# Kernel tuning notes

Measured on AMD Instinct MI355X. Metric: run time of the kernel, lower is better.

The kernel has to match this reference:

```python
import jax, jax.numpy as jnp
import numpy as np

LN_EPS = 1e-5
NORM_EPS = 1e-12


def channel_layernorm(x, w, b):
    # LayerNorm over channel dim of NCHW tensor (torch permutes to NHWC; equivalent)
    mu = x.mean(axis=1, keepdims=True)
    var = x.var(axis=1, keepdims=True)
    xn = (x - mu) / jnp.sqrt(var + LN_EPS)
    return xn * w[None, :, None, None] + b[None, :, None, None]


def pconv(x, w):
    # 1x1 pointwise conv, w: (out_ch, in_ch)
    return jnp.einsum('bchw,oc->bohw', x, w)


def dwconv3(x, w):
    # depthwise 3x3, padding 1; w: (ch, 1, 3, 3)
    return jax.lax.conv_general_dilated(
        x, w, window_strides=(1, 1), padding='SAME',
        feature_group_count=x.shape[1],
        dimension_numbers=('NCHW', 'OIHW', 'NCHW'))


def l2norm(x):
    n = jnp.sqrt(jnp.sum(x * x, axis=-1, keepdims=True))
    return x / jnp.maximum(n, NORM_EPS)


def setup_inputs() -> dict:
    key = jax.random.key(0)
    ks = jax.random.split(key, 8)
    B, C, H, W = 4, 128, 128, 128
    NH, G = 8, 2

    def w(k, shape, fan_in):
        return jax.random.normal(k, shape, dtype=jnp.float32) * (fan_in ** -0.5)

    return {
        'x': jax.random.normal(ks[0], (B, C, H, W), dtype=jnp.float32),
        'ln1_w': jnp.ones((C,), jnp.float32),
        'ln1_b': jnp.zeros((C,), jnp.float32),
        'temperature': jnp.ones((NH, 1, 1), jnp.float32),
        'qkv_p_w': w(ks[1], (3 * C, C), C),
        'qkv_d_w': w(ks[2], (3 * C, 1, 3, 3), 9),
        'proj_w': w(ks[3], (C, C), C),
        'ln2_w': jnp.ones((C,), jnp.float32),
        'ln2_b': jnp.zeros((C,), jnp.float32),
        'g1_w': w(ks[4], (2 * G * C, C), C),
        'gd_w': w(ks[5], (2 * G * C, 1, 3, 3), 9),
        'g2_w': w(ks[6], (C, G * C), G * C),
        'num_heads': NH,
    }


def reference(x, ln1_w, ln1_b, temperature, qkv_p_w, qkv_d_w, proj_w,
              ln2_w, ln2_b, g1_w, gd_w, g2_w, num_heads):
    b, c, h, w_ = x.shape
    d = c // num_heads

    # --- MDTA branch ---
    y = channel_layernorm(x, ln1_w, ln1_b)
    qkv = dwconv3(pconv(y, qkv_p_w), qkv_d_w)  # (b, 3c, h, w)
    q, k, v = jnp.split(qkv, 3, axis=1)
    q = l2norm(q.reshape(b, num_heads, d, h * w_))
    k = l2norm(k.reshape(b, num_heads, d, h * w_))
    v = v.reshape(b, num_heads, d, h * w_)
    # transposed (channel) attention: (b, heads, d, d)
    attn = jnp.einsum('bhdn,bhen->bhde', q, k) * temperature[None]
    attn = jax.nn.softmax(attn, axis=-1)
    out = jnp.einsum('bhde,bhen->bhdn', attn, v).reshape(b, c, h, w_)
    x = x + pconv(out, proj_w)

    # --- GDFN branch ---
    y = channel_layernorm(x, ln2_w, ln2_b)
    hdn = dwconv3(pconv(y, g1_w), gd_w)  # (b, 2*gamma*c, h, w)
    x1, x2 = jnp.split(hdn, 2, axis=1)
    g = jax.nn.gelu(x1, approximate=False) * x2
    x = x + pconv(g, g2_w)
    return x
```

## Files before the change

kernel.cpp:

```cpp
#include <hip/hip_runtime.h>
#include <cstdint>
#include <cstddef>

typedef float f32x4 __attribute__((ext_vector_type(4)));
typedef __bf16 bf16x8 __attribute__((ext_vector_type(8)));

__device__ __forceinline__ float b2f(unsigned short u) {
    union { unsigned int i; float f; } z; z.i = ((unsigned int)u) << 16; return z.f;
}
__device__ __forceinline__ unsigned short f2b(float f) {
    union { float f; unsigned int i; } z; z.f = f;
    unsigned int x = z.i;
    return (unsigned short)((x + 0x7FFFu + ((x >> 16) & 1u)) >> 16);
}

static constexpr int C = 128;
static constexpr int NP = 16384;
static constexpr int NH = 8;

struct Ptr11 { const float* p[11]; };
__constant__ int kWN[11]   = {128, 128, 8, 49152, 3456, 16384, 128, 128, 65536, 4608, 32768};
__constant__ int kWOff[11] = {0, 128, 256, 272, 49424, 52880, 69264, 69392, 69520, 135056, 139664};
static constexpr int kWTotal = 172432;

__global__ __launch_bounds__(256)
void cvt_w_kernel(Ptr11 P, unsigned short* __restrict__ dst)
{
    int seg = blockIdx.y;
    int n = kWN[seg];
    int i = blockIdx.x * 256 + threadIdx.x;
    if (i >= n) return;
    dst[kWOff[seg] + i] = f2b(P.p[seg][i]);
}

__global__ __launch_bounds__(256)
void ln_kernel(const float* __restrict__ x, const unsigned short* __restrict__ g,
               const unsigned short* __restrict__ beta, unsigned short* __restrict__ y)
{
    int wave = threadIdx.x >> 6;
    int lane = threadIdx.x & 63;
    int px   = lane & 15;
    int cgrp = lane >> 4;
    int pglob = blockIdx.x * 64 + wave * 16 + px;
    int b = pglob >> 14;
    int n = pglob & (NP - 1);
    const float* xb = x + (size_t)b * C * NP + n;

    float vals[32];
    float s = 0.f, s2 = 0.f;
    #pragma unroll
    for (int i = 0; i < 32; ++i) {
        float v = xb[(size_t)(cgrp + 4 * i) * NP];
        vals[i] = v;
        s += v; s2 += v * v;
    }
    s  += __shfl_xor(s, 16, 64);  s2 += __shfl_xor(s2, 16, 64);
    s  += __shfl_xor(s, 32, 64);  s2 += __shfl_xor(s2, 32, 64);
    float mu = s * (1.0f / C);
    float var = s2 * (1.0f / C) - mu * mu;
    float rs = rsqrtf(fmaxf(var, 0.f) + 1e-5f);

    unsigned short* yb = y + (size_t)b * C * NP + n;
    #pragma unroll
    for (int i = 0; i < 32; ++i) {
        int c = cgrp + 4 * i;
        float o = (vals[i] - mu) * rs * b2f(g[c]) + b2f(beta[c]);
        yb[(size_t)c * NP] = f2b(o);
    }
}

template <int K, int EPI>
__global__ __launch_bounds__(256)
void gemm_pconv(const unsigned short* __restrict__ W,
                const unsigned short* __restrict__ X,
                void* __restrict__ Out,
                const float* __restrict__ Res,
                int Cout)
{
    __shared__ unsigned short Bs[32][128];
    const int tid = threadIdx.x;
    const int b = blockIdx.z;
    const int n0 = blockIdx.x * 128;
    const int m0 = blockIdx.y * 128;
    const unsigned short* Xb = X + (size_t)b * K * NP;
    const int wid = tid >> 6;
    const int lane = tid & 63;
    const int ln16 = lane & 15;
    const int quad = lane >> 4;
    const int wy = wid >> 1;
    const int wx = wid & 1;

    f32x4 acc[4][4];
    #pragma unroll
    for (int i = 0; i < 4; ++i)
        #pragma unroll
        for (int j = 0; j < 4; ++j)
            acc[i][j] = f32x4{0.f, 0.f, 0.f, 0.f};

    for (int k0 = 0; k0 < K; k0 += 32) {
        #pragma unroll
        for (int r = 0; r < 2; ++r) {
            int flat = tid + r * 256;
            int kk = flat >> 4;
            int nn = (flat & 15) * 8;
            uint4 v = *(const uint4*)(Xb + (size_t)(k0 + kk) * NP + n0 + nn);
            *(uint4*)(&Bs[kk][nn]) = v;
        }
        __syncthreads();

        bf16x8 afr[4];
        #pragma unroll
        for (int mt = 0; mt < 4; ++mt) {
            int m = m0 + wy * 64 + mt * 16 + ln16;
            uint4 v = *(const uint4*)(W + (size_t)m * K + k0 + quad * 8);
            afr[mt] = *(bf16x8*)&v;
        }
        bf16x8 bfr[4];
        #pragma unroll
        for (int nt = 0; nt < 4; ++nt) {
            int n = wx * 64 + nt * 16 + ln16;
            union { bf16x8 v; unsigned short u[8]; } tmp;
            #pragma unroll
            for (int j = 0; j < 8; ++j) tmp.u[j] = Bs[quad * 8 + j][n];
            bfr[nt] = tmp.v;
        }
        #pragma unroll
        for (int mt = 0; mt < 4; ++mt)
            #pragma unroll
            for (int nt = 0; nt < 4; ++nt)
                acc[mt][nt] = __builtin_amdgcn_mfma_f32_16x16x32_bf16(
                    afr[mt], bfr[nt], acc[mt][nt], 0, 0, 0);
        __syncthreads();
    }

    size_t outbase = (size_t)b * Cout * NP;
    #pragma unroll
    for (int mt = 0; mt < 4; ++mt) {
        #pragma unroll
        for (int nt = 0; nt < 4; ++nt) {
            int co0 = m0 + wy * 64 + mt * 16 + quad * 4;
            int n = n0 + wx * 64 + nt * 16 + ln16;
            #pragma unroll
            for (int r = 0; r < 4; ++r) {
                float v = acc[mt][nt][r];
                size_t idx = outbase + (size_t)(co0 + r) * NP + n;
                if (EPI == 0) ((unsigned short*)Out)[idx] = f2b(v);
                else          ((float*)Out)[idx] = Res[idx] + v;
            }
        }
    }
}

__global__ __launch_bounds__(256)
void dwconv3_kernel(const unsigned short* __restrict__ in,
                    const unsigned short* __restrict__ w9,
                    unsigned short* __restrict__ out, int CH)
{
    int t = blockIdx.x * 256 + threadIdx.x;
    int xi = (t & 15) * 8;
    int y  = (t >> 4) & 127;
    int bc = t >> 11;
    int c  = bc % CH;
    const unsigned short* base = in + (size_t)bc * NP + y * 128 + xi;

    float wr[9];
    #pragma unroll
    for (int i = 0; i < 9; ++i) wr[i] = b2f(w9[c * 9 + i]);

    uint4 rv0 = uint4{0,0,0,0}, rv1, rv2 = uint4{0,0,0,0};
    if (y > 0)   rv0 = *(const uint4*)(base - 128);
    rv1 = *(const uint4*)(base);
    if (y < 127) rv2 = *(const uint4*)(base + 128);
    uint4 rows[3] = {rv0, rv1, rv2};

    float o[8];
    #pragma unroll
    for (int j = 0; j < 8; ++j) o[j] = 0.f;

    #pragma unroll
    for (int r = 0; r < 3; ++r) {
        union { uint4 v; unsigned short u[8]; } cv; cv.v = rows[r];
        int lh = __shfl_up((int)cv.u[7], 1, 16);
        int rh = __shfl_down((int)cv.u[0], 1, 16);
        float p[10];
        p[0] = (xi > 0)   ? b2f((unsigned short)lh) : 0.f;
        p[9] = (xi < 120) ? b2f((unsigned short)rh) : 0.f;
        #pragma unroll
        for (int j = 0; j < 8; ++j) p[j + 1] = b2f(cv.u[j]);
        #pragma unroll
        for (int j = 0; j < 8; ++j)
            o[j] += wr[r * 3] * p[j] + wr[r * 3 + 1] * p[j + 1] + wr[r * 3 + 2] * p[j + 2];
    }
    union { uint4 v; unsigned short u[8]; } res;
    #pragma unroll
    for (int j = 0; j < 8; ++j) res.u[j] = f2b(o[j]);
    *(uint4*)(out + (size_t)bc * NP + y * 128 + xi) = res.v;
}

__global__ __launch_bounds__(256)
void dwgelu_kernel(const unsigned short* __restrict__ hdn,
                   const unsigned short* __restrict__ w9,
                   unsigned short* __restrict__ g)
{
    int t = blockIdx.x * 256 + threadIdx.x;
    int xi = (t & 15) * 8;
    int y  = (t >> 4) & 127;
    int bc = t >> 11;
    int c  = bc & 255;
    int b  = bc >> 8;
    const unsigned short* base1 = hdn + ((size_t)b * 512 + c) * NP + y * 128 + xi;
    const unsigned short* base2 = base1 + (size_t)256 * NP;

    float w1[9], w2[9];
    #pragma unroll
    for (int i = 0; i < 9; ++i) {
        w1[i] = b2f(w9[c * 9 + i]);
        w2[i] = b2f(w9[(c + 256) * 9 + i]);
    }

    uint4 ra0 = uint4{0,0,0,0}, ra1, ra2 = uint4{0,0,0,0};
    uint4 rb0 = uint4{0,0,0,0}, rb1, rb2 = uint4{0,0,0,0};
    if (y > 0)   { ra0 = *(const uint4*)(base1 - 128); rb0 = *(const uint4*)(base2 - 128); }
    ra1 = *(const uint4*)(base1);
    rb1 = *(const uint4*)(base2);
    if (y < 127) { ra2 = *(const uint4*)(base1 + 128); rb2 = *(const uint4*)(base2 + 128); }
    uint4 rowsA[3] = {ra0, ra1, ra2};
    uint4 rowsB[3] = {rb0, rb1, rb2};

    float a1[8], a2[8];
    #pragma unroll
    for (int j = 0; j < 8; ++j) { a1[j] = 0.f; a2[j] = 0.f; }

    #pragma unroll
    for (int r = 0; r < 3; ++r) {
        union { uint4 v; unsigned short u[8]; } c1, c2;
        c1.v = rowsA[r]; c2.v = rowsB[r];
        int lh1 = __shfl_up((int)c1.u[7], 1, 16);
        int rh1 = __shfl_down((int)c1.u[0], 1, 16);
        int lh2 = __shfl_up((int)c2.u[7], 1, 16);
        int rh2 = __shfl_down((int)c2.u[0], 1, 16);
        float p1[10], p2[10];
        p1[0] = (xi > 0)   ? b2f((unsigned short)lh1) : 0.f;
        p1[9] = (xi < 120) ? b2f((unsigned short)rh1) : 0.f;
        p2[0] = (xi > 0)   ? b2f((unsigned short)lh2) : 0.f;
        p2[9] = (xi < 120) ? b2f((unsigned short)rh2) : 0.f;
        #pragma unroll
        for (int j = 0; j < 8; ++j) { p1[j + 1] = b2f(c1.u[j]); p2[j + 1] = b2f(c2.u[j]); }
        #pragma unroll
        for (int j = 0; j < 8; ++j) {
            a1[j] += w1[r * 3] * p1[j] + w1[r * 3 + 1] * p1[j + 1] + w1[r * 3 + 2] * p1[j + 2];
            a2[j] += w2[r * 3] * p2[j] + w2[r * 3 + 1] * p2[j + 1] + w2[r * 3 + 2] * p2[j + 2];
        }
    }
    union { uint4 v; unsigned short u[8]; } res;
    #pragma unroll
    for (int j = 0; j < 8; ++j) {
        float u = a1[j];
        float tt = u * (0.7978845608f + 0.0356774081f * u * u);
        float e = __expf(2.f * tt);
        float th = 1.f - 2.f / (e + 1.f);
        float ge = 0.5f * u * (1.f + th);
        res.u[j] = f2b(ge * a2[j]);
    }
    *(uint4*)(g + (size_t)bc * NP + y * 128 + xi) = res.v;
}

__global__ __launch_bounds__(256)
void sumsq_kernel(const unsigned short* __restrict__ qkv, float* __restrict__ norms)
{
    int ch = blockIdx.x;
    int b = blockIdx.y;
    const unsigned short* p = qkv + ((size_t)b * 384 + ch) * NP;
    float s = 0.f;
    for (int i = threadIdx.x * 8; i < NP; i += 2048) {
        union { uint4 v; unsigned short u[8]; } cv;
        cv.v = *(const uint4*)(p + i);
        #pragma unroll
        for (int j = 0; j < 8; ++j) { float v = b2f(cv.u[j]); s += v * v; }
    }
    #pragma unroll
    for (int o = 32; o > 0; o >>= 1) s += __shfl_down(s, o, 64);
    __shared__ float ws4[4];
    if ((threadIdx.x & 63) == 0) ws4[threadIdx.x >> 6] = s;
    __syncthreads();
    if (threadIdx.x == 0) {
        float t = ws4[0] + ws4[1] + ws4[2] + ws4[3];
        norms[b * 256 + ch] = fmaxf(sqrtf(t), 1e-12f);
    }
}

__global__ __launch_bounds__(256)
void gram_kernel(const unsigned short* __restrict__ qkv, float* __restrict__ Spart)
{
    int h = blockIdx.x, b = blockIdx.y, sp = blockIdx.z;
    int wid = threadIdx.x >> 6, lane = threadIdx.x & 63;
    int ln16 = lane & 15, quad = lane >> 4;
    int nbase = sp * 2048 + wid * 512;
    const unsigned short* qp = qkv + ((size_t)b * 384 + h * 16 + ln16) * NP;
    const unsigned short* kp = qkv + ((size_t)b * 384 + 128 + h * 16 + ln16) * NP;
    f32x4 acc = f32x4{0.f, 0.f, 0.f, 0.f};
    for (int i = 0; i < 512; i += 32) {
        int n = nbase + i + quad * 8;
        uint4 av = *(const uint4*)(qp + n);
        uint4 bv = *(const uint4*)(kp + n);
        acc = __builtin_amdgcn_mfma_f32_16x16x32_bf16(*(bf16x8*)&av, *(bf16x8*)&bv, acc, 0, 0, 0);
    }
    float* Sp = Spart + (((size_t)(b * NH + h) * 32) + sp * 4 + wid) * 256;
    #pragma unroll
    for (int r = 0; r < 4; ++r)
        Sp[(quad * 4 + r) * 16 + ln16] = acc[r];
}

__global__ __launch_bounds__(256)
void softmax_kernel(const float* __restrict__ Spart, const float* __restrict__ norms,
                    const unsigned short* __restrict__ temp, float* __restrict__ P)
{
    int bh = blockIdx.x;
    int b = bh >> 3, h = bh & 7;
    int t = threadIdx.x;
    int dq = t >> 4, dk = t & 15;
    float sacc = 0.f;
    const float* Sp = Spart + (size_t)bh * 32 * 256;
    #pragma unroll
    for (int j = 0; j < 32; ++j) sacc += Sp[j * 256 + t];
    float nq = norms[b * 256 + h * 16 + dq];
    float nk = norms[b * 256 + 128 + h * 16 + dk];
    float v = sacc / (nq * nk) * b2f(temp[h]);
    float m = v;
    #pragma unroll
    for (int o = 8; o > 0; o >>= 1) m = fmaxf(m, __shfl_xor(m, o, 16));
    float e = __expf(v - m);
    float s = e;
    #pragma unroll
    for (int o = 8; o > 0; o >>= 1) s += __shfl_xor(s, o, 16);
    P[(size_t)bh * 256 + t] = e / s;
}

__global__ __launch_bounds__(256)
void attnv_kernel(const float* __restrict__ P, const unsigned short* __restrict__ qkv,
                  unsigned short* __restrict__ out)
{
    __shared__ float Ps[256];
    int h = blockIdx.y, b = blockIdx.z;
    Ps[threadIdx.x] = P[((size_t)b * NH + h) * 256 + threadIdx.x];
    __syncthreads();
    int n = (blockIdx.x * 256 + threadIdx.x) * 4;
    const unsigned short* vp = qkv + ((size_t)b * 384 + 256 + h * 16) * NP + n;
    float o[16][4];
    #pragma unroll
    for (int d = 0; d < 16; ++d)
        #pragma unroll
        for (int j = 0; j < 4; ++j) o[d][j] = 0.f;
    #pragma unroll
    for (int e = 0; e < 16; ++e) {
        union { uint2 v; unsigned short u[4]; } cv;
        cv.v = *(const uint2*)(vp + (size_t)e * NP);
        float v0 = b2f(cv.u[0]), v1 = b2f(cv.u[1]), v2 = b2f(cv.u[2]), v3 = b2f(cv.u[3]);
        #pragma unroll
        for (int d = 0; d < 16; ++d) {
            float p = Ps[d * 16 + e];
            o[d][0] += p * v0; o[d][1] += p * v1; o[d][2] += p * v2; o[d][3] += p * v3;
        }
    }
    unsigned short* op = out + ((size_t)b * C + h * 16) * NP + n;
    #pragma unroll
    for (int d = 0; d < 16; ++d) {
        union { uint2 v; unsigned short u[4]; } res;
        #pragma unroll
        for (int j = 0; j < 4; ++j) res.u[j] = f2b(o[d][j]);
        *(uint2*)(op + (size_t)d * NP) = res.v;
    }
}

struct Bufs {
    float* xmid;
    unsigned short* y;
    unsigned short* big;
    unsigned short* mid;
    float* norms;
    float* Spart;
    float* P;
};

static void run_pipeline(const float* x_f32, float* out_f32,
                         const unsigned short* w,
                         const Bufs& B, int nb, hipStream_t stream)
{
    const unsigned short* ln1_w   = w + 0;
    const unsigned short* ln1_b   = w + 128;
    const unsigned short* temp    = w + 256;
    const unsigned short* qkv_p_w = w + 272;
    const unsigned short* qkv_d_w = w + 49424;
    const unsigned short* proj_w  = w + 52880;
    const unsigned short* ln2_w   = w + 69264;
    const unsigned short* ln2_b   = w + 69392;
    const unsigned short* g1_w    = w + 69520;
    const unsigned short* gd_w    = w + 135056;
    const unsigned short* g2_w    = w + 139664;

    ln_kernel<<<nb * NP / 64, 256, 0, stream>>>(x_f32, ln1_w, ln1_b, B.y);
    gemm_pconv<128, 0><<<dim3(NP / 128, 3, nb), 256, 0, stream>>>(qkv_p_w, B.y, B.big, nullptr, 384);
    dwconv3_kernel<<<nb * 384 * NP / 2048, 256, 0, stream>>>(B.big, qkv_d_w, B.mid, 384);
    sumsq_kernel<<<dim3(256, nb), 256, 0, stream>>>(B.mid, B.norms);
    gram_kernel<<<dim3(NH, nb, 8), 256, 0, stream>>>(B.mid, B.Spart);
    softmax_kernel<<<nb * NH, 256, 0, stream>>>(B.Spart, B.norms, temp, B.P);
    attnv_kernel<<<dim3(NP / 1024, NH, nb), 256, 0, stream>>>(B.P, B.mid, B.y);
    gemm_pconv<128, 1><<<dim3(NP / 128, 1, nb), 256, 0, stream>>>(proj_w, B.y, B.xmid, x_f32, 128);

    ln_kernel<<<nb * NP / 64, 256, 0, stream>>>(B.xmid, ln2_w, ln2_b, B.y);
    gemm_pconv<128, 0><<<dim3(NP / 128, 4, nb), 256, 0, stream>>>(g1_w, B.y, B.big, nullptr, 512);
    dwgelu_kernel<<<nb * 256 * NP / 2048, 256, 0, stream>>>(B.big, gd_w, B.mid);
    gemm_pconv<256, 1><<<dim3(NP / 128, 1, nb), 256, 0, stream>>>(g2_w, B.mid, out_f32, B.xmid, 128);
}

extern "C" void kernel_launch(void* const* d_in, const int* in_sizes, int n_in,
                              void* d_out, int out_size, void* d_ws, size_t ws_size,
                              hipStream_t stream)
{
    (void)in_sizes; (void)n_in; (void)out_size;
    const float* x = (const float*)d_in[0];
    char* ws = (char*)d_ws;

    size_t off = 0;
    unsigned short* wpack = (unsigned short*)(ws + off);
    off += (size_t)kWTotal * 2;
    off = (off + 255) & ~(size_t)255;
    size_t header = off;

    auto layout = [&](int nb, size_t o, Bufs& B) -> size_t {
        B.xmid = (float*)(ws + o);           o += (size_t)nb * C * NP * 4;
        B.y    = (unsigned short*)(ws + o);  o += (size_t)nb * C * NP * 2;
        B.big  = (unsigned short*)(ws + o);  o += (size_t)nb * 512 * NP * 2;
        B.mid  = (unsigned short*)(ws + o);  o += (size_t)nb * 384 * NP * 2;
        B.norms = (float*)(ws + o);          o += (size_t)nb * 256 * 4;
        B.Spart = (float*)(ws + o);          o += (size_t)nb * NH * 32 * 256 * 4;
        B.P     = (float*)(ws + o);          o += (size_t)nb * NH * 256 * 4;
        return o;
    };

    Ptr11 P;
    for (int i = 0; i < 11; ++i) P.p[i] = (const float*)d_in[i + 1];
    cvt_w_kernel<<<dim3(256, 11), 256, 0, stream>>>(P, wpack);

    Bufs Bfull;
    size_t need_full = layout(4, header, Bfull);

    if (ws_size >= need_full) {
        run_pipeline(x, (float*)d_out, wpack, Bfull, 4, stream);
    } else {
        Bufs B1;
        layout(1, header, B1);
        for (int b = 0; b < 4; ++b) {
            run_pipeline(x + (size_t)b * C * NP,
                         (float*)d_out + (size_t)b * C * NP,
                         wpack, B1, 1, stream);
        }
    }
}
```

Before: 275.5 us.

## Switch LN and attention outputs to pixel-major layout and fuse sum-of-squares into dwconv

```diff
diff --git a/kernel.cpp b/kernel.cpp
--- a/kernel.cpp
+++ b/kernel.cpp
@@ -33,49 +33,147 @@
     dst[kWOff[seg] + i] = f2b(P.p[seg][i]);
 }
 
+__global__ void zero_kernel(float* __restrict__ p) { p[blockIdx.x * 256 + threadIdx.x] = 0.f; }
+
 __global__ __launch_bounds__(256)
 void ln_kernel(const float* __restrict__ x, const unsigned short* __restrict__ g,
                const unsigned short* __restrict__ beta, unsigned short* __restrict__ y)
 {
-    int wave = threadIdx.x >> 6;
-    int lane = threadIdx.x & 63;
-    int px   = lane & 15;
-    int cgrp = lane >> 4;
-    int pglob = blockIdx.x * 64 + wave * 16 + px;
+    int t = threadIdx.x;
+    int px = t & 15;
+    int tg = t >> 4;
+    int pglob = blockIdx.x * 16 + px;
     int b = pglob >> 14;
     int n = pglob & (NP - 1);
     const float* xb = x + (size_t)b * C * NP + n;
 
-    float vals[32];
-    float s = 0.f, s2 = 0.f;
-    #pragma unroll
-    for (int i = 0; i < 32; ++i) {
-        float v = xb[(size_t)(cgrp + 4 * i) * NP];
-        vals[i] = v;
-        s += v; s2 += v * v;
+    float v[8]; float s = 0.f, s2 = 0.f;
+    #pragma unroll
+    for (int i = 0; i < 8; ++i) {
+        float w = xb[(size_t)(tg * 8 + i) * NP];
+        v[i] = w; s += w; s2 += w * w;
     }
     s  += __shfl_xor(s, 16, 64);  s2 += __shfl_xor(s2, 16, 64);
     s  += __shfl_xor(s, 32, 64);  s2 += __shfl_xor(s2, 32, 64);
-    float mu = s * (1.0f / C);
-    float var = s2 * (1.0f / C) - mu * mu;
+    __shared__ float sm[2][4][16];
+    if ((t & 63) < 16) { sm[0][t >> 6][px] = s; sm[1][t >> 6][px] = s2; }
+    __syncthreads();
+    float S  = sm[0][0][px] + sm[0][1][px] + sm[0][2][px] + sm[0][3][px];
+    float S2 = sm[1][0][px] + sm[1][1][px] + sm[1][2][px] + sm[1][3][px];
+    float mu = S * (1.0f / C);
+    float var = S2 * (1.0f / C) - mu * mu;
     float rs = rsqrtf(fmaxf(var, 0.f) + 1e-5f);
 
-    unsigned short* yb = y + (size_t)b * C * NP + n;
-    #pragma unroll
-    for (int i = 0; i < 32; ++i) {
-        int c = cgrp + 4 * i;
-        float o = (vals[i] - mu) * rs * b2f(g[c]) + b2f(beta[c]);
-        yb[(size_t)c * NP] = f2b(o);
-    }
+    union { uint4 q; unsigned short u[8]; } res;
+    #pragma unroll
+    for (int i = 0; i < 8; ++i) {
+        int c = tg * 8 + i;
+        res.u[i] = f2b((v[i] - mu) * rs * b2f(g[c]) + b2f(beta[c]));
+    }
+    *(uint4*)(y + (size_t)pglob * C + tg * 8) = res.q;
 }
 
 template <int K, int EPI>
 __global__ __launch_bounds__(256)
-void gemm_pconv(const unsigned short* __restrict__ W,
-                const unsigned short* __restrict__ X,
-                void* __restrict__ Out,
-                const float* __restrict__ Res,
-                int Cout)
+void gemm_nk(const unsigned short* __restrict__ W,
+             const unsigned short* __restrict__ X,
+             void* __restrict__ Out,
+             const float* __restrict__ Res,
+             int Cout)
+{
+    const int tid = threadIdx.x;
+    const int b = blockIdx.z;
+    const int n0 = blockIdx.x * 128;
+    const int co0 = blockIdx.y * 128;
+    const int lane = tid & 63;
+    const int wid = tid >> 6;
+    const int ln16 = lane & 15;
+    const int quad = lane >> 4;
+    const int wy = wid >> 1;
+    const int wx = wid & 1;
+    const unsigned short* Xb = X + ((size_t)b * NP + n0) * K;
+
+    f32x4 acc[4][4];
+    #pragma unroll
+    for (int i = 0; i < 4; ++i)
+        #pragma unroll
+        for (int j = 0; j < 4; ++j)
+            acc[i][j] = f32x4{0.f, 0.f, 0.f, 0.f};
+
+    #pragma unroll 2
+    for (int k0 = 0; k0 < K; k0 += 32) {
+        bf16x8 afr[4];
+        #pragma unroll
+        for (int mt = 0; mt < 4; ++mt) {
+            int row = wy * 64 + mt * 16 + ln16;
+            uint4 v = *(const uint4*)(Xb + (size_t)row * K + k0 + quad * 8);
+            afr[mt] = *(bf16x8*)&v;
+        }
+        bf16x8 bfr[4];
+        #pragma unroll
+        for (int nt = 0; nt < 4; ++nt) {
+            int co = co0 + wx * 64 + nt * 16 + ln16;
+            uint4 v = *(const uint4*)(W + (size_t)co * K + k0 + quad * 8);
+            bfr[nt] = *(bf16x8*)&v;
+        }
+        #pragma unroll
+        for (int mt = 0; mt < 4; ++mt)
+            #pragma unroll
+            for (int nt = 0; nt < 4; ++nt)
+                acc[mt][nt] = __builtin_amdgcn_mfma_f32_16x16x32_bf16(
+                    afr[mt], bfr[nt], acc[mt][nt], 0, 0, 0);
+    }
+
+    if constexpr (EPI == 0) {
+        __shared__ unsigned short Ts[128 * 136];
+        #pragma unroll
+        for (int mt = 0; mt < 4; ++mt) {
+            #pragma unroll
+            for (int nt = 0; nt < 4; ++nt) {
+                int co_l = wx * 64 + nt * 16 + ln16;
+                int n_l  = wy * 64 + mt * 16 + quad * 4;
+                union { uint2 d; unsigned short u[4]; } pk;
+                #pragma unroll
+                for (int r = 0; r < 4; ++r) pk.u[r] = f2b(acc[mt][nt][r]);
+                *(uint2*)&Ts[co_l * 136 + n_l] = pk.d;
+            }
+        }
+        __syncthreads();
+        unsigned short* ob = (unsigned short*)Out;
+        #pragma unroll
+        for (int i = 0; i < 8; ++i) {
+            int idx = tid + 256 * i;
+            int co_l = idx >> 4;
+            int oct  = idx & 15;
+            uint4 v = *(const uint4*)&Ts[co_l * 136 + oct * 8];
+            *(uint4*)(ob + (size_t)b * Cout * NP + (size_t)(co0 + co_l) * NP + n0 + oct * 8) = v;
+        }
+    } else {
+        float* ob = (float*)Out;
+        #pragma unroll
+        for (int mt = 0; mt < 4; ++mt) {
+            #pragma unroll
+            for (int nt = 0; nt < 4; ++nt) {
+                int co = co0 + wx * 64 + nt * 16 + ln16;
+                int n = n0 + wy * 64 + mt * 16 + quad * 4;
+                size_t idx = (size_t)b * Cout * NP + (size_t)co * NP + n;
+                f32x4 rv = *(const f32x4*)&Res[idx];
+                f32x4 ov;
+                #pragma unroll
+                for (int r = 0; r < 4; ++r) ov[r] = rv[r] + acc[mt][nt][r];
+                *(f32x4*)&ob[idx] = ov;
+            }
+        }
+    }
+}
+
+template <int K>
+__global__ __launch_bounds__(256)
+void gemm_cn(const unsigned short* __restrict__ W,
+             const unsigned short* __restrict__ X,
+             float* __restrict__ Out,
+             const float* __restrict__ Res,
+             int Cout)
 {
     __shared__ unsigned short Bs[32][128];
     const int tid = threadIdx.x;
@@ -133,7 +231,6 @@
         __syncthreads();
     }
 
-    size_t outbase = (size_t)b * Cout * NP;
     #pragma unroll
     for (int mt = 0; mt < 4; ++mt) {
         #pragma unroll
@@ -142,10 +239,8 @@
             int n = n0 + wx * 64 + nt * 16 + ln16;
             #pragma unroll
             for (int r = 0; r < 4; ++r) {
-                float v = acc[mt][nt][r];
-                size_t idx = outbase + (size_t)(co0 + r) * NP + n;
-                if (EPI == 0) ((unsigned short*)Out)[idx] = f2b(v);
-                else          ((float*)Out)[idx] = Res[idx] + v;
+                size_t idx = (size_t)b * Cout * NP + (size_t)(co0 + r) * NP + n;
+                Out[idx] = Res[idx] + acc[mt][nt][r];
             }
         }
     }
@@ -154,13 +249,15 @@
 __global__ __launch_bounds__(256)
 void dwconv3_kernel(const unsigned short* __restrict__ in,
                     const unsigned short* __restrict__ w9,
-                    unsigned short* __restrict__ out, int CH)
+                    unsigned short* __restrict__ out, int CH,
+                    float* __restrict__ norms2)
 {
     int t = blockIdx.x * 256 + threadIdx.x;
     int xi = (t & 15) * 8;
     int y  = (t >> 4) & 127;
     int bc = t >> 11;
     int c  = bc % CH;
+    int b  = bc / CH;
     const unsigned short* base = in + (size_t)bc * NP + y * 128 + xi;
 
     float wr[9];
@@ -192,9 +289,18 @@
             o[j] += wr[r * 3] * p[j] + wr[r * 3 + 1] * p[j + 1] + wr[r * 3 + 2] * p[j + 2];
     }
     union { uint4 v; unsigned short u[8]; } res;
-    #pragma unroll
-    for (int j = 0; j < 8; ++j) res.u[j] = f2b(o[j]);
+    float ss = 0.f;
+    #pragma unroll
+    for (int j = 0; j < 8; ++j) { res.u[j] = f2b(o[j]); ss += o[j] * o[j]; }
     *(uint4*)(out + (size_t)bc * NP + y * 128 + xi) = res.v;
+
+    #pragma unroll
+    for (int off = 32; off > 0; off >>= 1) ss += __shfl_down(ss, off, 64);
+    __shared__ float sred[4];
+    if ((threadIdx.x & 63) == 0) sred[threadIdx.x >> 6] = ss;
+    __syncthreads();
+    if (threadIdx.x == 0 && c < 256)
+        atomicAdd(&norms2[b * 256 + c], sred[0] + sred[1] + sred[2] + sred[3]);
 }
 
 __global__ __launch_bounds__(256)
@@ -259,34 +365,9 @@
         float tt = u * (0.7978845608f + 0.0356774081f * u * u);
         float e = __expf(2.f * tt);
         float th = 1.f - 2.f / (e + 1.f);
-        float ge = 0.5f * u * (1.f + th);
-        res.u[j] = f2b(ge * a2[j]);
+        res.u[j] = f2b(0.5f * u * (1.f + th) * a2[j]);
     }
     *(uint4*)(g + (size_t)bc * NP + y * 128 + xi) = res.v;
-}
-
-__global__ __launch_bounds__(256)
-void sumsq_kernel(const unsigned short* __restrict__ qkv, float* __restrict__ norms)
-{
-    int ch = blockIdx.x;
-    int b = blockIdx.y;
-    const unsigned short* p = qkv + ((size_t)b * 384 + ch) * NP;
-    float s = 0.f;
-    for (int i = threadIdx.x * 8; i < NP; i += 2048) {
-        union { uint4 v; unsigned short u[8]; } cv;
-        cv.v = *(const uint4*)(p + i);
-        #pragma unroll
-        for (int j = 0; j < 8; ++j) { float v = b2f(cv.u[j]); s += v * v; }
-    }
-    #pragma unroll
-    for (int o = 32; o > 0; o >>= 1) s += __shfl_down(s, o, 64);
-    __shared__ float ws4[4];
-    if ((threadIdx.x & 63) == 0) ws4[threadIdx.x >> 6] = s;
-    __syncthreads();
-    if (threadIdx.x == 0) {
-        float t = ws4[0] + ws4[1] + ws4[2] + ws4[3];
-        norms[b * 256 + ch] = fmaxf(sqrtf(t), 1e-12f);
-    }
 }
 
 __global__ __launch_bounds__(256)
@@ -312,7 +393,7 @@
 }
 
 __global__ __launch_bounds__(256)
-void softmax_kernel(const float* __restrict__ Spart, const float* __restrict__ norms,
+void softmax_kernel(const float* __restrict__ Spart, const float* __restrict__ norms2,
                     const unsigned short* __restrict__ temp, float* __restrict__ P)
 {
     int bh = blockIdx.x;
@@ -323,8 +404,8 @@
     const float* Sp = Spart + (size_t)bh * 32 * 256;
     #pragma unroll
     for (int j = 0; j < 32; ++j) sacc += Sp[j * 256 + t];
-    float nq = norms[b * 256 + h * 16 + dq];
-    float nk = norms[b * 256 + 128 + h * 16 + dk];
+    float nq = fmaxf(sqrtf(norms2[b * 256 + h * 16 + dq]), 1e-12f);
+    float nk = fmaxf(sqrtf(norms2[b * 256 + 128 + h * 16 + dk]), 1e-12f);
     float v = sacc / (nq * nk) * b2f(temp[h]);
     float m = v;
     #pragma unroll
@@ -344,8 +425,8 @@
     int h = blockIdx.y, b = blockIdx.z;
     Ps[threadIdx.x] = P[((size_t)b * NH + h) * 256 + threadIdx.x];
     __syncthreads();
-    int n = (blockIdx.x * 256 + threadIdx.x) * 4;
-    const unsigned short* vp = qkv + ((size_t)b * 384 + 256 + h * 16) * NP + n;
+    int n0 = (blockIdx.x * 256 + threadIdx.x) * 4;
+    const unsigned short* vp = qkv + ((size_t)b * 384 + 256 + h * 16) * NP + n0;
     float o[16][4];
     #pragma unroll
     for (int d = 0; d < 16; ++d)
@@ -362,13 +443,14 @@
             o[d][0] += p * v0; o[d][1] += p * v1; o[d][2] += p * v2; o[d][3] += p * v3;
         }
     }
-    unsigned short* op = out + ((size_t)b * C + h * 16) * NP + n;
-    #pragma unroll
-    for (int d = 0; d < 16; ++d) {
-        union { uint2 v; unsigned short u[4]; } res;
-        #pragma unroll
-        for (int j = 0; j < 4; ++j) res.u[j] = f2b(o[d][j]);
-        *(uint2*)(op + (size_t)d * NP) = res.v;
+    #pragma unroll
+    for (int j = 0; j < 4; ++j) {
+        union { uint4 q[2]; unsigned short u[16]; } res;
+        #pragma unroll
+        for (int d = 0; d < 16; ++d) res.u[d] = f2b(o[d][j]);
+        unsigned short* op = out + ((size_t)b * NP + n0 + j) * 128 + h * 16;
+        *(uint4*)op = res.q[0];
+        *(uint4*)(op + 8) = res.q[1];
     }
 }
 
@@ -377,14 +459,13 @@
     unsigned short* y;
     unsigned short* big;
     unsigned short* mid;
-    float* norms;
+    float* norms2;
     float* Spart;
     float* P;
 };
 
 static void run_pipeline(const float* x_f32, float* out_f32,
-                         const unsigned short* w,
-                         const Bufs& B, int nb, hipStream_t stream)
+                         const unsigned short* w, const Bufs& B, int nb, hipStream_t stream)
 {
     const unsigned short* ln1_w   = w + 0;
     const unsigned short* ln1_b   = w + 128;
@@ -398,19 +479,19 @@
     const unsigned short* gd_w    = w + 135056;
     const unsigned short* g2_w    = w + 139664;
 
-    ln_kernel<<<nb * NP / 64, 256, 0, stream>>>(x_f32, ln1_w, ln1_b, B.y);
-    gemm_pconv<128, 0><<<dim3(NP / 128, 3, nb), 256, 0, stream>>>(qkv_p_w, B.y, B.big, nullptr, 384);
-    dwconv3_kernel<<<nb * 384 * NP / 2048, 256, 0, stream>>>(B.big, qkv_d_w, B.mid, 384);
-    sumsq_kernel<<<dim3(256, nb), 256, 0, stream>>>(B.mid, B.norms);
+    ln_kernel<<<nb * NP / 16, 256, 0, stream>>>(x_f32, ln1_w, ln1_b, B.y);
+    gemm_nk<128, 0><<<dim3(NP / 128, 3, nb), 256, 0, stream>>>(qkv_p_w, B.y, B.big, nullptr, 384);
+    zero_kernel<<<nb, 256, 0, stream>>>(B.norms2);
+    dwconv3_kernel<<<nb * 384 * NP / 2048, 256, 0, stream>>>(B.big, qkv_d_w, B.mid, 384, B.norms2);
     gram_kernel<<<dim3(NH, nb, 8), 256, 0, stream>>>(B.mid, B.Spart);
-    softmax_kernel<<<nb * NH, 256, 0, stream>>>(B.Spart, B.norms, temp, B.P);
+    softmax_kernel<<<nb * NH, 256, 0, stream>>>(B.Spart, B.norms2, temp, B.P);
     attnv_kernel<<<dim3(NP / 1024, NH, nb), 256, 0, stream>>>(B.P, B.mid, B.y);
-    gemm_pconv<128, 1><<<dim3(NP / 128, 1, nb), 256, 0, stream>>>(proj_w, B.y, B.xmid, x_f32, 128);
-
-    ln_kernel<<<nb * NP / 64, 256, 0, stream>>>(B.xmid, ln2_w, ln2_b, B.y);
-    gemm_pconv<128, 0><<<dim3(NP / 128, 4, nb), 256, 0, stream>>>(g1_w, B.y, B.big, nullptr, 512);
+    gemm_nk<128, 1><<<dim3(NP / 128, 1, nb), 256, 0, stream>>>(proj_w, B.y, B.xmid, x_f32, 128);
+
+    ln_kernel<<<nb * NP / 16, 256, 0, stream>>>(B.xmid, ln2_w, ln2_b, B.y);
+    gemm_nk<128, 0><<<dim3(NP / 128, 4, nb), 256, 0, stream>>>(g1_w, B.y, B.big, nullptr, 512);
     dwgelu_kernel<<<nb * 256 * NP / 2048, 256, 0, stream>>>(B.big, gd_w, B.mid);
-    gemm_pconv<256, 1><<<dim3(NP / 128, 1, nb), 256, 0, stream>>>(g2_w, B.mid, out_f32, B.xmid, 128);
+    gemm_cn<256><<<dim3(NP / 128, 1, nb), 256, 0, stream>>>(g2_w, B.mid, out_f32, B.xmid, 128);
 }
 
 extern "C" void kernel_launch(void* const* d_in, const int* in_sizes, int n_in,
@@ -432,9 +513,9 @@
         B.y    = (unsigned short*)(ws + o);  o += (size_t)nb * C * NP * 2;
         B.big  = (unsigned short*)(ws + o);  o += (size_t)nb * 512 * NP * 2;
         B.mid  = (unsigned short*)(ws + o);  o += (size_t)nb * 384 * NP * 2;
-        B.norms = (float*)(ws + o);          o += (size_t)nb * 256 * 4;
-        B.Spart = (float*)(ws + o);          o += (size_t)nb * NH * 32 * 256 * 4;
-        B.P     = (float*)(ws + o);          o += (size_t)nb * NH * 256 * 4;
+        B.norms2 = (float*)(ws + o);         o += (size_t)nb * 256 * 4;
+        B.Spart  = (float*)(ws + o);         o += (size_t)nb * NH * 32 * 256 * 4;
+        B.P      = (float*)(ws + o);         o += (size_t)nb * NH * 256 * 4;
         return o;
     };
 
```

After: 308.4 us. 11.9% more time.
